# Kernel tuning notes

Measured on AMD Instinct MI355X. Metric: run time of the kernel, lower is better.

The kernel has to match this reference:

```python
import jax, jax.numpy as jnp
import numpy as np

B, S, D = 4, 2048, 1024
H, DK, DV = 16, 64, 64
NEG = -1e10


def setup_inputs() -> dict:
    key = jax.random.key(0)
    ks = jax.random.split(key, 7)
    queries = jax.random.normal(ks[0], (B, S, D), dtype=jnp.float32)
    keys = jax.random.normal(ks[1], (B, S, D), dtype=jnp.float32)
    values = jax.random.normal(ks[2], (B, S, D), dtype=jnp.float32)
    mask = jnp.ones((B, S, S), dtype=jnp.int32)
    # per-head Linear weights, torch layout [out, in]; stacked over heads
    Wq = jax.random.normal(ks[3], (H, DK, D), dtype=jnp.float32) / np.sqrt(D)
    Wk = jax.random.normal(ks[4], (H, DK, D), dtype=jnp.float32) / np.sqrt(D)
    Wv = jax.random.normal(ks[5], (H, DV, D), dtype=jnp.float32) / np.sqrt(D)
    Wo = jax.random.normal(ks[6], (D, H * DV), dtype=jnp.float32) / np.sqrt(H * DV)
    return {"queries": queries, "keys": keys, "values": values, "mask": mask,
            "Wq": Wq, "Wk": Wk, "Wv": Wv, "Wo": Wo}


def reference(queries, keys, values, mask, Wq, Wk, Wv, Wo):
    # per-head projections, vectorized over heads: y = x @ W_h^T
    q = jnp.einsum('bsd,hkd->bhsk', queries, Wq)   # [B,H,S,DK]
    k = jnp.einsum('btd,hkd->bhtk', keys, Wk)      # [B,H,S,DK]
    v = jnp.einsum('btd,hvd->bhtv', values, Wv)    # [B,H,S,DV]
    scores = jnp.einsum('bhsk,bhtk->bhst', q, k) / jnp.sqrt(jnp.asarray(DK, q.dtype))
    scores = jnp.where(mask[:, None, :, :] == 0, jnp.asarray(NEG, q.dtype), scores)
    attn = jax.nn.softmax(scores, axis=-1)
    out = jnp.einsum('bhst,bhtv->bhsv', attn, v)   # [B,H,S,DV]
    # torch.cat over heads on last dim == head-major concat per position
    out = out.transpose(0, 2, 1, 3).reshape(B, S, H * DV)
    return out @ Wo.T
```

## Files before the change

kernel.cpp:

```cpp
#include <hip/hip_runtime.h>
#include <stdint.h>

typedef __attribute__((ext_vector_type(4))) float f32x4;
typedef __attribute__((ext_vector_type(8))) __bf16 bf16x8;
typedef __attribute__((ext_vector_type(4))) __bf16 bf16x4;
typedef __attribute__((ext_vector_type(4))) short s16x4;
typedef __attribute__((ext_vector_type(2))) uint32_t u32x2;

#define MFMA16(a, b, c) __builtin_amdgcn_mfma_f32_16x16x32_bf16(a, b, c, 0, 0, 0)
#define MFMA16K16(a, b, c) __builtin_amdgcn_mfma_f32_16x16x16bf16_1k(a, b, c, 0, 0, 0)

#define B_ 4
#define S_ 2048
#define D_ 1024
#define H_ 16
#define NEG_ -1e10f
#define QSCALE 0.180336880f
#define MNEG_ -100.0f

__device__ __forceinline__ float ex2(float x) { return __builtin_amdgcn_exp2f(x); }

__device__ __forceinline__ void glds16(const void* gsrc, void* ldst) {
  __builtin_amdgcn_global_load_lds(
      (__attribute__((address_space(1))) void*)(gsrc),
      (__attribute__((address_space(3))) void*)(ldst),
      16, 0, 0);
}

__device__ __forceinline__ uint32_t pack_bf16(float a, float b) {
  uint32_t ua = (uint32_t)__builtin_bit_cast(unsigned short, (__bf16)a);
  uint32_t ub = (uint32_t)__builtin_bit_cast(unsigned short, (__bf16)b);
  return ua | (ub << 16);
}

__global__ __launch_bounds__(256) void prep(
    const float* __restrict__ xq, const float* __restrict__ xk, const float* __restrict__ xv,
    const float* __restrict__ wq, const float* __restrict__ wk, const float* __restrict__ wv,
    const float* __restrict__ wo,
    __bf16* __restrict__ oxq, __bf16* __restrict__ oxk, __bf16* __restrict__ oxv,
    __bf16* __restrict__ owq, __bf16* __restrict__ owk, __bf16* __restrict__ owv,
    __bf16* __restrict__ owo,
    const int* __restrict__ mask, uint32_t* __restrict__ bits, int* __restrict__ flags) {
  int bid = blockIdx.x, tid = threadIdx.x;
  if (bid < 1536) {
    int z = bid >> 9, local = bid & 511;
    const float* in = (z == 0) ? xq : (z == 1) ? xk : xv;
    __bf16* out = (z == 0) ? oxq : (z == 1) ? oxk : oxv;
    #pragma unroll
    for (int it = 0; it < 16; it++) {
      size_t i4 = (size_t)(local * 256 + tid) + (size_t)it * (512 * 256);
      float4 v = *(const float4*)(in + i4 * 4);
      bf16x4 o;
      o.x = (__bf16)v.x; o.y = (__bf16)v.y; o.z = (__bf16)v.z; o.w = (__bf16)v.w;
      *(bf16x4*)(out + i4 * 4) = o;
    }
  } else if (bid < 1792) {
    int m = bid - 1536;
    int z = m >> 6, local = m & 63;
    const float* in = (z == 0) ? wq : (z == 1) ? wk : (z == 2) ? wv : wo;
    __bf16* out = (z == 0) ? owq : (z == 1) ? owk : (z == 2) ? owv : owo;
    #pragma unroll
    for (int it = 0; it < 16; it++) {
      size_t i4 = (size_t)(local * 256 + tid) + (size_t)it * (64 * 256);
      float4 v = *(const float4*)(in + i4 * 4);
      bf16x4 o;
      o.x = (__bf16)v.x; o.y = (__bf16)v.y; o.z = (__bf16)v.z; o.w = (__bf16)v.w;
      *(bf16x4*)(out + i4 * 4) = o;
    }
  } else {
    int wid = (bid - 1792) * 256 + tid;
    int word = wid & 63, grow = wid >> 6;
    const int* mp = mask + (size_t)grow * S_ + word * 32;
    uint32_t wbits = 0;
    #pragma unroll
    for (int j = 0; j < 8; j++) {
      int4 mv = *(const int4*)(mp + j * 4);
      wbits |= (mv.x != 0 ? 1u : 0u) << (j * 4);
      wbits |= (mv.y != 0 ? 1u : 0u) << (j * 4 + 1);
      wbits |= (mv.z != 0 ? 1u : 0u) << (j * 4 + 2);
      wbits |= (mv.w != 0 ? 1u : 0u) << (j * 4 + 3);
    }
    bits[(size_t)grow * 64 + word] = wbits;
    if (wbits != 0xFFFFFFFFu) {
      int b = grow >> 11, srow = grow & 2047;
      atomicAnd(&flags[(b * 16 + (srow >> 7)) * 16 + (word >> 2)], 0);
    }
  }
}

template <int MODE>
__global__ __launch_bounds__(256, 3) void gemm_bt(
    const __bf16* __restrict__ A0, const __bf16* __restrict__ A1, const __bf16* __restrict__ A2,
    const __bf16* __restrict__ W0, const __bf16* __restrict__ W1, const __bf16* __restrict__ W2,
    void* O0, void* O1, void* O2) {
  const int K = 1024;
  int lin = blockIdx.y * 8 + blockIdx.x;
  int swz = (lin & 7) * 64 + (lin >> 3);
  int bx = swz & 7, by = swz >> 3;

  const __bf16* PA; const __bf16* PB; void* O;
  int pa_t, pb_t;
  if (MODE == 0) {
    if (blockIdx.z == 0)      { PA = W0; PB = A0; O = O0; pa_t = bx; pb_t = by; }
    else if (blockIdx.z == 1) { PA = W1; PB = A1; O = O1; pa_t = bx; pb_t = by; }
    else                      { PA = A2; PB = W2; O = O2; pa_t = by; pb_t = bx; }
  } else { PA = W0; PB = A0; O = O0; pa_t = bx; pb_t = by; }

  __shared__ __align__(16) __bf16 As[128 * 64];
  __shared__ __align__(16) __bf16 Bs[128 * 64];
  int tid = threadIdx.x, lane = tid & 63, w = tid >> 6;
  int wm = w >> 1, wn = w & 1;
  int g = lane >> 4, l15 = lane & 15;
  f32x4 acc[4][4] = {};
  const __bf16* Ablk = PA + (size_t)(pa_t * 128) * K;
  const __bf16* Bblk = PB + (size_t)(pb_t * 128) * K;

  for (int kt = 0; kt < K; kt += 64) {
    __syncthreads();
    #pragma unroll
    for (int r = 0; r < 4; r++) {
      int C = r * 256 + tid;
      int row = C >> 3, c = C & 7;
      int c0 = c ^ (row & 7);
      glds16(Ablk + (size_t)row * K + kt + c0 * 8, (char*)As + C * 16);
      glds16(Bblk + (size_t)row * K + kt + c0 * 8, (char*)Bs + C * 16);
    }
    __syncthreads();
    #pragma unroll
    for (int kkq = 0; kkq < 2; kkq++) {
      bf16x8 af[4], bfr[4];
      #pragma unroll
      for (int i = 0; i < 4; i++) {
        int row = wm * 64 + i * 16 + l15;
        int ch = (kkq * 4 + g) ^ (row & 7);
        af[i] = *(const bf16x8*)((const char*)As + row * 128 + ch * 16);
      }
      #pragma unroll
      for (int j = 0; j < 4; j++) {
        int row = wn * 64 + j * 16 + l15;
        int ch = (kkq * 4 + g) ^ (row & 7);
        bfr[j] = *(const bf16x8*)((const char*)Bs + row * 128 + ch * 16);
      }
      #pragma unroll
      for (int i = 0; i < 4; i++)
        #pragma unroll
        for (int j = 0; j < 4; j++)
          acc[i][j] = MFMA16(af[i], bfr[j], acc[i][j]);
    }
  }

  if (MODE == 1) {
    #pragma unroll
    for (int i = 0; i < 4; i++)
      #pragma unroll
      for (int j = 0; j < 4; j++) {
        int n0 = pa_t * 128 + wm * 64 + i * 16 + g * 4;
        int m = pb_t * 128 + wn * 64 + j * 16 + l15;
        *(f32x4*)((float*)O + (size_t)m * 1024 + n0) = acc[i][j];
      }
  } else if (blockIdx.z == 2) {
    #pragma unroll
    for (int i = 0; i < 4; i++)
      #pragma unroll
      for (int j = 0; j < 4; j++) {
        int s0 = pa_t * 128 + wm * 64 + i * 16 + g * 4;
        int dvg = pb_t * 128 + wn * 64 + j * 16 + l15;
        int b = s0 >> 11, s = s0 & 2047;
        int h = dvg >> 6, dv = dvg & 63;
        bf16x4 o;
        #pragma unroll
        for (int r = 0; r < 4; r++) o[r] = (__bf16)acc[i][j][r];
        *(bf16x4*)((__bf16*)O + (((size_t)b * 16 + h) * 64 + dv) * 2048 + s) = o;
      }
  } else {
    float scale = (blockIdx.z == 0) ? QSCALE : 1.0f;
    #pragma unroll
    for (int i = 0; i < 4; i++)
      #pragma unroll
      for (int j = 0; j < 4; j++) {
        int dkg = pa_t * 128 + wm * 64 + i * 16 + g * 4;
        int sg = pb_t * 128 + wn * 64 + j * 16 + l15;
        int h = dkg >> 6, dk = dkg & 63;
        int b = sg >> 11, s = sg & 2047;
        bf16x4 o;
        #pragma unroll
        for (int r = 0; r < 4; r++) o[r] = (__bf16)(acc[i][j][r] * scale);
        *(bf16x4*)((__bf16*)O + (((size_t)b * 16 + h) * 2048 + s) * 64 + dk) = o;
      }
  }
}

__global__ __launch_bounds__(256, 4) void attn(
    const __bf16* __restrict__ qp, const __bf16* __restrict__ kp,
    const __bf16* __restrict__ vt_, __bf16* __restrict__ aout,
    const uint32_t* __restrict__ bits, const int* __restrict__ flags) {
  int lin = blockIdx.y * 16 + blockIdx.x;
  int swz = (lin & 7) * 128 + (lin >> 3);
  int qt = swz & 15, bh = swz >> 4;
  int b = bh >> 4, h = bh & 15;
  int tid = threadIdx.x, lane = tid & 63, w = tid >> 6;
  int g = lane >> 4, l15 = lane & 15;
  int hs0 = ((g & 1) ^ ((l15 >> 3) & 1)) * 8;

  __shared__ __align__(16) char smem[32768];

  const __bf16* Qg = qp + ((size_t)bh * S_ + qt * 128) * 64;
  const __bf16* Kg = kp + (size_t)bh * S_ * 64;
  const __bf16* Vg = vt_ + (size_t)bh * 64 * S_;

  #pragma unroll
  for (int r = 0; r < 4; r++) {
    int C = r * 256 + tid;
    int row = C >> 3, c = C & 7, c0 = c ^ (row & 7);
    glds16(Qg + row * 64 + c0 * 8, smem + C * 16);
  }
  __syncthreads();
  bf16x8 qf[2][2];
  #pragma unroll
  for (int i = 0; i < 2; i++)
    #pragma unroll
    for (int kkq = 0; kkq < 2; kkq++) {
      int row = w * 32 + i * 16 + l15;
      int ch = (kkq * 4 + g) ^ (row & 7);
      qf[i][kkq] = *(const bf16x8*)(smem + row * 128 + ch * 16);
    }
  __syncthreads();

  auto stageK = [&](int kt2, int p) {
    char* Kl = smem + p * 16384;
    const __bf16* Ks = Kg + (size_t)kt2 * 64 * 64;
    #pragma unroll
    for (int r = 0; r < 2; r++) {
      int C = r * 256 + tid;
      int row = C >> 3, c = C & 7, c0 = c ^ (row & 7);
      glds16(Ks + (size_t)row * 64 + c0 * 8, Kl + C * 16);
    }
  };
  auto loadV = [&](int kt2, int4* vreg) {
    #pragma unroll
    for (int r = 0; r < 2; r++) {
      int C = r * 256 + tid;
      int row = C >> 3, c = C & 7;
      int c0 = c ^ (row & 7);
      vreg[r] = *(const int4*)(Vg + (size_t)row * S_ + kt2 * 64 + c0 * 8);
    }
  };
  auto writeV = [&](int p, const int4* vreg) {
    char* Vl = smem + p * 16384 + 8192;
    #pragma unroll
    for (int r = 0; r < 2; r++) {
      int C = r * 256 + tid;
      int row = C >> 3;
      int4 v = vreg[r];
      bool sw = (row & 8) != 0;
      int4 wv;
      wv.x = sw ? v.z : v.x; wv.y = sw ? v.w : v.y;
      wv.z = sw ? v.x : v.z; wv.w = sw ? v.y : v.w;
      *(int4*)(Vl + C * 16) = wv;
    }
  };

  f32x4 oacc[4][2] = {};
  f32x4 sumacc[2] = {};
  const f32x4 zero4 = {0.f, 0.f, 0.f, 0.f};
  const s16x4 ones = {(short)0x3F80, (short)0x3F80, (short)0x3F80, (short)0x3F80};

  int4 vreg[2];

  stageK(0, 0);
  loadV(0, vreg);
  asm volatile("s_waitcnt vmcnt(0)" ::: "memory");
  writeV(0, vreg);
  asm volatile("s_waitcnt lgkmcnt(0)" ::: "memory");
  __builtin_amdgcn_s_barrier();
  __builtin_amdgcn_sched_barrier(0);

  for (int kt = 0; kt < 32; kt++) {
    int cur = kt & 1;
    if (kt + 1 < 32) {
      stageK(kt + 1, cur ^ 1);
      loadV(kt + 1, vreg);
    }
    __builtin_amdgcn_sched_barrier(0);

    const char* Klds = smem + cur * 16384;
    const char* Vlds = Klds + 8192;
    int fl = flags[(b * 16 + qt) * 16 + (kt >> 1)];

    f32x4 sacc[2][4];
    __builtin_amdgcn_s_setprio(1);
    #pragma unroll
    for (int jt = 0; jt < 4; jt++) {
      int row = jt * 16 + l15;
      bf16x8 kf0 = *(const bf16x8*)(Klds + row * 128 + (g ^ (row & 7)) * 16);
      bf16x8 kf1 = *(const bf16x8*)(Klds + row * 128 + ((4 + g) ^ (row & 7)) * 16);
      sacc[0][jt] = MFMA16(kf0, qf[0][0], zero4);
      sacc[0][jt] = MFMA16(kf1, qf[0][1], sacc[0][jt]);
      sacc[1][jt] = MFMA16(kf0, qf[1][0], zero4);
      sacc[1][jt] = MFMA16(kf1, qf[1][1], sacc[1][jt]);
    }
    __builtin_amdgcn_s_setprio(0);

    if (!fl) {
      #pragma unroll
      for (int i = 0; i < 2; i++) {
        int srow = qt * 128 + w * 32 + i * 16 + l15;
        const uint32_t* bw = &bits[((size_t)b * S_ + srow) * 64 + kt * 2];
        uint32_t mw[2] = {bw[0], bw[1]};
        #pragma unroll
        for (int jt = 0; jt < 4; jt++)
          #pragma unroll
          for (int r = 0; r < 4; r++) {
            int bitpos = (jt & 1) * 16 + g * 4 + r;
            if (!((mw[jt >> 1] >> bitpos) & 1)) sacc[i][jt][r] = MNEG_;
          }
      }
    }

    #pragma unroll
    for (int jt = 0; jt < 4; jt++) {
      s16x4 pf[2];
      #pragma unroll
      for (int i = 0; i < 2; i++) {
        float p0 = ex2(sacc[i][jt][0]);
        float p1 = ex2(sacc[i][jt][1]);
        float p2 = ex2(sacc[i][jt][2]);
        float p3 = ex2(sacc[i][jt][3]);
        u32x2 t;
        t.x = pack_bf16(p0, p1);
        t.y = pack_bf16(p2, p3);
        pf[i] = __builtin_bit_cast(s16x4, t);
      }
      int ch = jt * 2 + (g >> 1);
      __builtin_amdgcn_s_setprio(1);
      #pragma unroll
      for (int vt = 0; vt < 4; vt++) {
        int row = vt * 16 + l15;
        int chs = ch ^ (row & 7);
        s16x4 vv = *(const s16x4*)(Vlds + row * 128 + chs * 16 + hs0);
        oacc[vt][0] = MFMA16K16(vv, pf[0], oacc[vt][0]);
        oacc[vt][1] = MFMA16K16(vv, pf[1], oacc[vt][1]);
      }
      sumacc[0] = MFMA16K16(ones, pf[0], sumacc[0]);
      sumacc[1] = MFMA16K16(ones, pf[1], sumacc[1]);
      __builtin_amdgcn_s_setprio(0);
    }

    asm volatile("s_waitcnt vmcnt(0)" ::: "memory");
    if (kt + 1 < 32) writeV(cur ^ 1, vreg);
    asm volatile("s_waitcnt lgkmcnt(0)" ::: "memory");
    __builtin_amdgcn_s_barrier();
    __builtin_amdgcn_sched_barrier(0);
  }

  #pragma unroll
  for (int i = 0; i < 2; i++) {
    float inv = 1.0f / sumacc[i][0];
    int srow = qt * 128 + w * 32 + i * 16 + l15;
    #pragma unroll
    for (int vt = 0; vt < 4; vt++) {
      bf16x4 o;
      #pragma unroll
      for (int r = 0; r < 4; r++) o[r] = (__bf16)(oacc[vt][i][r] * inv);
      *(bf16x4*)(aout + ((size_t)b * S_ + srow) * 1024 + h * 64 + vt * 16 + g * 4) = o;
    }
  }
}

extern "C" void kernel_launch(void* const* d_in, const int* in_sizes, int n_in,
                              void* d_out, int out_size, void* d_ws, size_t ws_size,
                              hipStream_t stream) {
  const float* queries = (const float*)d_in[0];
  const float* keys    = (const float*)d_in[1];
  const float* values  = (const float*)d_in[2];
  const int*   mask    = (const int*)d_in[3];
  const float* Wq      = (const float*)d_in[4];
  const float* Wk      = (const float*)d_in[5];
  const float* Wv      = (const float*)d_in[6];
  const float* Wo      = (const float*)d_in[7];

  char* ws = (char*)d_ws;
  __bf16* Xq  = (__bf16*)(ws + 0);
  __bf16* Xk  = (__bf16*)(ws + 16777216);
  __bf16* Xv  = (__bf16*)(ws + 33554432);
  __bf16* Wqb = (__bf16*)(ws + 50331648);
  __bf16* Wkb = (__bf16*)(ws + 52428800);
  __bf16* Wvb = (__bf16*)(ws + 54525952);
  __bf16* Wob = (__bf16*)(ws + 56623104);
  __bf16* qp  = (__bf16*)(ws + 58720256);
  __bf16* kp  = (__bf16*)(ws + 75497472);
  __bf16* vT  = (__bf16*)(ws + 92274688);
  uint32_t* bits = (uint32_t*)(ws + 109051904);
  int* flags     = (int*)(ws + 111149056);
  __bf16* aout = Xq;

  hipMemsetAsync(flags, 0xFF, 4096, stream);

  prep<<<3840, 256, 0, stream>>>(queries, keys, values, Wq, Wk, Wv, Wo,
                                 Xq, Xk, Xv, Wqb, Wkb, Wvb, Wob,
                                 mask, bits, flags);

  gemm_bt<0><<<dim3(8, 64, 3), 256, 0, stream>>>(Xq, Xk, Xv, Wqb, Wkb, Wvb,
                                                 (void*)qp, (void*)kp, (void*)vT);

  attn<<<dim3(16, 64), 256, 0, stream>>>(qp, kp, vT, aout, bits, flags);

  gemm_bt<1><<<dim3(8, 64, 1), 256, 0, stream>>>(aout, nullptr, nullptr, Wob, nullptr, nullptr,
                                                 (void*)d_out, nullptr, nullptr);
}
```

Before: 384.4 us.

## Use K=32 bf16 MFMA for PV product with permuted V staging layout

```diff
diff --git a/kernel.cpp b/kernel.cpp
--- a/kernel.cpp
+++ b/kernel.cpp
@@ -6,9 +6,9 @@
 typedef __attribute__((ext_vector_type(4))) __bf16 bf16x4;
 typedef __attribute__((ext_vector_type(4))) short s16x4;
 typedef __attribute__((ext_vector_type(2))) uint32_t u32x2;
+typedef __attribute__((ext_vector_type(4))) uint32_t u32x4;
 
 #define MFMA16(a, b, c) __builtin_amdgcn_mfma_f32_16x16x32_bf16(a, b, c, 0, 0, 0)
-#define MFMA16K16(a, b, c) __builtin_amdgcn_mfma_f32_16x16x16bf16_1k(a, b, c, 0, 0, 0)
 
 #define B_ 4
 #define S_ 2048
@@ -200,7 +200,6 @@
   int b = bh >> 4, h = bh & 15;
   int tid = threadIdx.x, lane = tid & 63, w = tid >> 6;
   int g = lane >> 4, l15 = lane & 15;
-  int hs0 = ((g & 1) ^ ((l15 >> 3) & 1)) * 8;
 
   __shared__ __align__(16) char smem[32768];
 
@@ -240,9 +239,14 @@
     #pragma unroll
     for (int r = 0; r < 2; r++) {
       int C = r * 256 + tid;
-      int row = C >> 3, c = C & 7;
-      int c0 = c ^ (row & 7);
-      vreg[r] = *(const int4*)(Vg + (size_t)row * S_ + kt2 * 64 + c0 * 8);
+      int row = C >> 3, sc = C & 7;
+      int p16 = sc ^ (row & 7);
+      int t2 = p16 >> 2, g4 = p16 & 3;
+      const __bf16* src = Vg + (size_t)row * S_ + kt2 * 64 + t2 * 32 + g4 * 4;
+      int2 lo = *(const int2*)(src);
+      int2 hi = *(const int2*)(src + 16);
+      int4 v; v.x = lo.x; v.y = lo.y; v.z = hi.x; v.w = hi.y;
+      vreg[r] = v;
     }
   };
   auto writeV = [&](int p, const int4* vreg) {
@@ -250,20 +254,15 @@
     #pragma unroll
     for (int r = 0; r < 2; r++) {
       int C = r * 256 + tid;
-      int row = C >> 3;
-      int4 v = vreg[r];
-      bool sw = (row & 8) != 0;
-      int4 wv;
-      wv.x = sw ? v.z : v.x; wv.y = sw ? v.w : v.y;
-      wv.z = sw ? v.x : v.z; wv.w = sw ? v.y : v.w;
-      *(int4*)(Vl + C * 16) = wv;
+      *(int4*)(Vl + C * 16) = vreg[r];
     }
   };
 
   f32x4 oacc[4][2] = {};
   f32x4 sumacc[2] = {};
   const f32x4 zero4 = {0.f, 0.f, 0.f, 0.f};
-  const s16x4 ones = {(short)0x3F80, (short)0x3F80, (short)0x3F80, (short)0x3F80};
+  const u32x4 ones_u = {0x3F803F80u, 0x3F803F80u, 0x3F803F80u, 0x3F803F80u};
+  const bf16x8 ones8 = __builtin_bit_cast(bf16x8, ones_u);
 
   int4 vreg[2];
 
@@ -318,31 +317,36 @@
     }
 
     #pragma unroll
-    for (int jt = 0; jt < 4; jt++) {
-      s16x4 pf[2];
+    for (int t2 = 0; t2 < 2; t2++) {
+      bf16x8 pf[2];
       #pragma unroll
       for (int i = 0; i < 2; i++) {
-        float p0 = ex2(sacc[i][jt][0]);
-        float p1 = ex2(sacc[i][jt][1]);
-        float p2 = ex2(sacc[i][jt][2]);
-        float p3 = ex2(sacc[i][jt][3]);
-        u32x2 t;
-        t.x = pack_bf16(p0, p1);
-        t.y = pack_bf16(p2, p3);
-        pf[i] = __builtin_bit_cast(s16x4, t);
-      }
-      int ch = jt * 2 + (g >> 1);
+        float a0 = ex2(sacc[i][2 * t2][0]);
+        float a1 = ex2(sacc[i][2 * t2][1]);
+        float a2 = ex2(sacc[i][2 * t2][2]);
+        float a3 = ex2(sacc[i][2 * t2][3]);
+        float b0 = ex2(sacc[i][2 * t2 + 1][0]);
+        float b1 = ex2(sacc[i][2 * t2 + 1][1]);
+        float b2 = ex2(sacc[i][2 * t2 + 1][2]);
+        float b3 = ex2(sacc[i][2 * t2 + 1][3]);
+        u32x4 t;
+        t.x = pack_bf16(a0, a1);
+        t.y = pack_bf16(a2, a3);
+        t.z = pack_bf16(b0, b1);
+        t.w = pack_bf16(b2, b3);
+        pf[i] = __builtin_bit_cast(bf16x8, t);
+      }
       __builtin_amdgcn_s_setprio(1);
       #pragma unroll
       for (int vt = 0; vt < 4; vt++) {
         int row = vt * 16 + l15;
-        int chs = ch ^ (row & 7);
-        s16x4 vv = *(const s16x4*)(Vlds + row * 128 + chs * 16 + hs0);
-        oacc[vt][0] = MFMA16K16(vv, pf[0], oacc[vt][0]);
-        oacc[vt][1] = MFMA16K16(vv, pf[1], oacc[vt][1]);
-      }
-      sumacc[0] = MFMA16K16(ones, pf[0], sumacc[0]);
-      sumacc[1] = MFMA16K16(ones, pf[1], sumacc[1]);
+        int c16 = (t2 * 4 + g) ^ (row & 7);
+        bf16x8 vv = *(const bf16x8*)(Vlds + row * 128 + c16 * 16);
+        oacc[vt][0] = MFMA16(vv, pf[0], oacc[vt][0]);
+        oacc[vt][1] = MFMA16(vv, pf[1], oacc[vt][1]);
+      }
+      sumacc[0] = MFMA16(ones8, pf[0], sumacc[0]);
+      sumacc[1] = MFMA16(ones8, pf[1], sumacc[1]);
       __builtin_amdgcn_s_setprio(0);
     }
 
```

Result: faster. 357.5 us (-7.0%).
